# Performance work log

Hardware: AMD Instinct MI355X
Metric: run time of the kernel (lower is better)

The kernel has to match this reference:

```python
import jax, jax.numpy as jnp
import numpy as np

HIDDEN = 20
VOCAB = 29
NUM_LAYERS = 1
SEQ_LEN = 64
BATCH = 16384


def setup_inputs() -> dict:
    key = jax.random.key(0)
    k1, k2, k3, k4, k5 = jax.random.split(key, 5)
    return {
        "x": jax.random.normal(k1, (SEQ_LEN, BATCH, VOCAB), dtype=jnp.float32),
        "img_emb": jax.random.normal(k2, (BATCH, HIDDEN), dtype=jnp.float32),
        "W_ih": jax.random.normal(k3, (NUM_LAYERS, HIDDEN, VOCAB), dtype=jnp.float32),
        "b_ih": jnp.zeros((NUM_LAYERS, HIDDEN), dtype=jnp.float32),
        "W_hh": jax.random.normal(k4, (NUM_LAYERS, HIDDEN, HIDDEN), dtype=jnp.float32),
        "b_hh": jnp.zeros((NUM_LAYERS, HIDDEN), dtype=jnp.float32),
        "W_ho": jax.random.normal(k5, (VOCAB, HIDDEN), dtype=jnp.float32),
        "b_ho": jnp.zeros((VOCAB,), dtype=jnp.float32),
    }


def reference(x, img_emb, W_ih, b_ih, W_hh, b_hh, W_ho, b_ho):
    # num_layers == 1: take layer 0 weights
    Wi, bi = W_ih[0], b_ih[0]   # [H,V], [H]
    Wh, bh = W_hh[0], b_hh[0]   # [H,H], [H]
    seq_len, batch = x.shape[0], x.shape[1]
    # img_emb is only added at t == 0
    first = (jnp.arange(seq_len) == 0).astype(x.dtype)  # [T]

    def step(h, inp):
        xt, f = inp  # xt: [B,V], f: scalar
        h_new = jnp.tanh(xt @ Wi.T + bi + h @ Wh.T + bh + f * img_emb)
        return h_new, h_new

    h0 = jnp.zeros((batch, Wi.shape[0]), dtype=x.dtype)
    _, hs = jax.lax.scan(step, h0, (x, first))  # hs: [T,B,H]
    logits = hs @ W_ho.T + b_ho  # [T,B,V]
    return jax.nn.log_softmax(logits, axis=-1)
```

## Files before the change

kernel.cpp:

```cpp
#include <hip/hip_runtime.h>

#define Tn 64
#define Bn 16384
#define Vn 29
#define Hn 20

typedef float f4 __attribute__((ext_vector_type(4)));

static __device__ __forceinline__ f4 ld4u(const float* p) {
  f4 v; __builtin_memcpy(&v, p, 16); return v;
}
static __device__ __forceinline__ void st4u(float* p, f4 v) {
  __builtin_memcpy(p, &v, 16);
}

#define LOG2E 1.4426950408889634f
#define LN2   0.6931471805599453f

static __device__ __forceinline__ float frcp(float x) {
#if __has_builtin(__builtin_amdgcn_rcpf)
  return __builtin_amdgcn_rcpf(x);
#else
  return 1.0f / x;
#endif
}
static __device__ __forceinline__ float fexp2(float x) {
#if __has_builtin(__builtin_amdgcn_exp2f)
  return __builtin_amdgcn_exp2f(x);
#else
  return exp2f(x);
#endif
}
static __device__ __forceinline__ float flog2(float x) {
#if __has_builtin(__builtin_amdgcn_logf)
  return __builtin_amdgcn_logf(x);
#else
  return log2f(x);
#endif
}
static __device__ __forceinline__ float ftanh(float x) {
  float e = fexp2(x * (2.0f * LOG2E));
  return 1.0f - 2.0f * frcp(1.0f + e);
}

#define SWZ(v, imm) __int_as_float(__builtin_amdgcn_ds_swizzle(__float_as_int(v), (imm)))
#define PAT(ow) (((ow) << 5) | 0x18)

__global__ __launch_bounds__(256, 3) void k_pre(
    const float* __restrict__ x, const float* __restrict__ img,
    const float* __restrict__ Wi, const float* __restrict__ bih,
    const float* __restrict__ bhh, float* __restrict__ xi)
{
  __shared__ f4 sW[Hn * 8];
  __shared__ float sB[Hn];
  float* sWf = (float*)sW;
  const int tid = threadIdx.x;
  for (int i = tid; i < Hn * 32; i += 256) {
    int r = i >> 5, c = i & 31;
    sWf[i] = (c < Vn) ? Wi[r * Vn + c] : 0.0f;
  }
  if (tid < Hn) sB[tid] = bih[tid] + bhh[tid];
  __syncthreads();

  const int g  = blockIdx.x * 256 + tid;
  const int t  = g >> 13;
  const int b0 = (g & 8191) << 1;

  const float* xr = x + ((size_t)t * Bn + b0) * Vn;
  f4 xa[8], xb[8];
#pragma unroll
  for (int q = 0; q < 7; ++q) {
    xa[q] = ld4u(xr + 4 * q);
    xb[q] = ld4u(xr + Vn + 4 * q);
  }
  xa[7] = f4{xr[28], 0.0f, 0.0f, 0.0f};
  xb[7] = f4{xr[Vn + 28], 0.0f, 0.0f, 0.0f};

  const bool first = (t == 0);
  const float* ia = img + (size_t)b0 * Hn;
  float* orow = xi + ((size_t)t * Bn + b0) * Hn;

  float oa4[4], ob4[4];
#pragma unroll
  for (int h = 0; h < Hn; ++h) {
    float aa = sB[h], ab = sB[h];
#pragma unroll
    for (int q = 0; q < 8; ++q) {
      f4 w = sW[h * 8 + q];
      aa += w.x * xa[q].x + w.y * xa[q].y + w.z * xa[q].z + w.w * xa[q].w;
      ab += w.x * xb[q].x + w.y * xb[q].y + w.z * xb[q].z + w.w * xb[q].w;
    }
    if (first) { aa += ia[h]; ab += ia[Hn + h]; }
    oa4[h & 3] = aa; ob4[h & 3] = ab;
    if ((h & 3) == 3) {
      *(f4*)(orow + (h - 3))      = f4{oa4[0], oa4[1], oa4[2], oa4[3]};
      *(f4*)(orow + Hn + (h - 3)) = f4{ob4[0], ob4[1], ob4[2], ob4[3]};
    }
  }
}

__global__ __launch_bounds__(256, 2) void k_rnn(
    const float* __restrict__ xi, const float* __restrict__ Wh,
    const float* __restrict__ Who, const float* __restrict__ bho,
    float* __restrict__ out)
{
  const int gt = blockIdx.x * 256 + threadIdx.x;
  const int b = gt >> 3;
  const int j = gt & 7;

  float wh[3][Hn];
#pragma unroll
  for (int s = 0; s < 3; ++s) {
    int r = 3 * j + s; r = r > 19 ? 19 : r;
    const f4* wr = (const f4*)(Wh + r * Hn);
#pragma unroll
    for (int q = 0; q < 5; ++q) {
      f4 v = wr[q];
      wh[s][4*q] = v.x; wh[s][4*q+1] = v.y; wh[s][4*q+2] = v.z; wh[s][4*q+3] = v.w;
    }
  }
  float wo[4][Hn], bo[4];
#pragma unroll
  for (int rr = 0; rr < 4; ++rr) {
    int v = 4 * j + rr; int vc = v > 28 ? 28 : v;
    const f4* wr = (const f4*)(Who + vc * Hn);
#pragma unroll
    for (int q = 0; q < 5; ++q) {
      f4 w = wr[q];
      wo[rr][4*q] = w.x; wo[rr][4*q+1] = w.y; wo[rr][4*q+2] = w.z; wo[rr][4*q+3] = w.w;
    }
    bo[rr] = (v < Vn) ? bho[v] : -1e30f;
  }

  int c0 = 3 * j;     c0 = c0 > 19 ? 19 : c0;
  int c1 = 3 * j + 1; c1 = c1 > 19 ? 19 : c1;
  int c2 = 3 * j + 2; c2 = c2 > 19 ? 19 : c2;

  const float* xp = xi + (size_t)b * Hn;
  float nx0 = xp[c0], nx1 = xp[c1], nx2 = xp[c2];

  float hbc[Hn];
#pragma unroll
  for (int k = 0; k < Hn; ++k) hbc[k] = 0.0f;

  float* op = out + (size_t)b * Vn + 4 * j;
  const size_t xstep = (size_t)Bn * Hn;
  const size_t ostep = (size_t)Bn * Vn;

#pragma unroll 1
  for (int t = 0; t < Tn; ++t) {
    float a0 = nx0, a1 = nx1, a2 = nx2;
    xp += xstep;
    nx0 = xp[c0]; nx1 = xp[c1]; nx2 = xp[c2];

#pragma unroll
    for (int k = 0; k < Hn; ++k) {
      float hk = hbc[k];
      a0 += hk * wh[0][k]; a1 += hk * wh[1][k]; a2 += hk * wh[2][k];
    }
    float h0 = ftanh(a0), h1 = ftanh(a1), h2 = ftanh(a2);

    hbc[0]  = SWZ(h0, PAT(0)); hbc[1]  = SWZ(h1, PAT(0)); hbc[2]  = SWZ(h2, PAT(0));
    hbc[3]  = SWZ(h0, PAT(1)); hbc[4]  = SWZ(h1, PAT(1)); hbc[5]  = SWZ(h2, PAT(1));
    hbc[6]  = SWZ(h0, PAT(2)); hbc[7]  = SWZ(h1, PAT(2)); hbc[8]  = SWZ(h2, PAT(2));
    hbc[9]  = SWZ(h0, PAT(3)); hbc[10] = SWZ(h1, PAT(3)); hbc[11] = SWZ(h2, PAT(3));
    hbc[12] = SWZ(h0, PAT(4)); hbc[13] = SWZ(h1, PAT(4)); hbc[14] = SWZ(h2, PAT(4));
    hbc[15] = SWZ(h0, PAT(5)); hbc[16] = SWZ(h1, PAT(5)); hbc[17] = SWZ(h2, PAT(5));
    hbc[18] = SWZ(h0, PAT(6)); hbc[19] = SWZ(h1, PAT(6));

    float l0 = bo[0], l1 = bo[1], l2 = bo[2], l3 = bo[3];
#pragma unroll
    for (int k = 0; k < Hn; ++k) {
      float hk = hbc[k];
      l0 += hk * wo[0][k]; l1 += hk * wo[1][k];
      l2 += hk * wo[2][k]; l3 += hk * wo[3][k];
    }

    float m = fmaxf(fmaxf(l0, l1), fmaxf(l2, l3));
    m = fmaxf(m, SWZ(m, 0x041F));
    m = fmaxf(m, SWZ(m, 0x081F));
    m = fmaxf(m, SWZ(m, 0x101F));
    float e0 = fexp2((l0 - m) * LOG2E), e1 = fexp2((l1 - m) * LOG2E);
    float e2 = fexp2((l2 - m) * LOG2E), e3 = fexp2((l3 - m) * LOG2E);
    float s = e0 + e1 + e2 + e3;
    s += SWZ(s, 0x041F);
    s += SWZ(s, 0x081F);
    s += SWZ(s, 0x101F);
    float ls = m + flog2(s) * LN2;

    f4 o = f4{l0 - ls, l1 - ls, l2 - ls, l3 - ls};
    if (j < 7) st4u(op, o);
    else       op[0] = l0 - ls;
    op += ostep;
  }
}

extern "C" void kernel_launch(void* const* d_in, const int* in_sizes, int n_in,
                              void* d_out, int out_size, void* d_ws, size_t ws_size,
                              hipStream_t stream)
{
  const float* x   = (const float*)d_in[0];
  const float* img = (const float*)d_in[1];
  const float* Wi  = (const float*)d_in[2];
  const float* bi  = (const float*)d_in[3];
  const float* Wh  = (const float*)d_in[4];
  const float* bh  = (const float*)d_in[5];
  const float* Who = (const float*)d_in[6];
  const float* bho = (const float*)d_in[7];
  float* out = (float*)d_out;
  float* xi  = (float*)d_ws;

  k_pre<<<(Tn * Bn / 2) / 256, 256, 0, stream>>>(x, img, Wi, bi, bh, xi);
  k_rnn<<<(8 * Bn) / 256, 256, 0, stream>>>(xi, Wh, Who, bho, out);
}
```

Baseline: 316.1 us.

## Fuse input projection into recurrent kernel with prefetched x rows and swizzle broadcast

Removes the separate pre-projection kernel and its workspace round trip. The recurrent kernel now loads raw x rows, with each of the 8 lanes per batch row holding a 4-element slice. It computes x·Wi^T by broadcasting x elements through ds_swizzle, adds the biases and the image embedding at t=0, and prefetches x three steps ahead. This saves writing and rereading the 64×B×20 intermediate, but adds 29 swizzles and 87 FMAs per step on the serial recurrence path, more register pressure (launch bounds lowered to 1), and fewer waves in flight.

```diff
diff --git a/kernel.cpp b/kernel.cpp
--- a/kernel.cpp
+++ b/kernel.cpp
@@ -46,61 +46,31 @@
 #define SWZ(v, imm) __int_as_float(__builtin_amdgcn_ds_swizzle(__float_as_int(v), (imm)))
 #define PAT(ow) (((ow) << 5) | 0x18)
 
-__global__ __launch_bounds__(256, 3) void k_pre(
-    const float* __restrict__ x, const float* __restrict__ img,
-    const float* __restrict__ Wi, const float* __restrict__ bih,
-    const float* __restrict__ bhh, float* __restrict__ xi)
-{
-  __shared__ f4 sW[Hn * 8];
-  __shared__ float sB[Hn];
-  float* sWf = (float*)sW;
-  const int tid = threadIdx.x;
-  for (int i = tid; i < Hn * 32; i += 256) {
-    int r = i >> 5, c = i & 31;
-    sWf[i] = (c < Vn) ? Wi[r * Vn + c] : 0.0f;
-  }
-  if (tid < Hn) sB[tid] = bih[tid] + bhh[tid];
-  __syncthreads();
-
-  const int g  = blockIdx.x * 256 + tid;
-  const int t  = g >> 13;
-  const int b0 = (g & 8191) << 1;
-
-  const float* xr = x + ((size_t)t * Bn + b0) * Vn;
-  f4 xa[8], xb[8];
-#pragma unroll
-  for (int q = 0; q < 7; ++q) {
-    xa[q] = ld4u(xr + 4 * q);
-    xb[q] = ld4u(xr + Vn + 4 * q);
-  }
-  xa[7] = f4{xr[28], 0.0f, 0.0f, 0.0f};
-  xb[7] = f4{xr[Vn + 28], 0.0f, 0.0f, 0.0f};
-
-  const bool first = (t == 0);
-  const float* ia = img + (size_t)b0 * Hn;
-  float* orow = xi + ((size_t)t * Bn + b0) * Hn;
-
-  float oa4[4], ob4[4];
-#pragma unroll
-  for (int h = 0; h < Hn; ++h) {
-    float aa = sB[h], ab = sB[h];
-#pragma unroll
-    for (int q = 0; q < 8; ++q) {
-      f4 w = sW[h * 8 + q];
-      aa += w.x * xa[q].x + w.y * xa[q].y + w.z * xa[q].z + w.w * xa[q].w;
-      ab += w.x * xb[q].x + w.y * xb[q].y + w.z * xb[q].z + w.w * xb[q].w;
-    }
-    if (first) { aa += ia[h]; ab += ia[Hn + h]; }
-    oa4[h & 3] = aa; ob4[h & 3] = ab;
-    if ((h & 3) == 3) {
-      *(f4*)(orow + (h - 3))      = f4{oa4[0], oa4[1], oa4[2], oa4[3]};
-      *(f4*)(orow + Hn + (h - 3)) = f4{ob4[0], ob4[1], ob4[2], ob4[3]};
-    }
-  }
-}
-
-__global__ __launch_bounds__(256, 2) void k_rnn(
-    const float* __restrict__ xi, const float* __restrict__ Wh,
+#define XI_STEP(xv, c) { \
+  float xb_ = SWZ((xv)[(c) & 3], PAT((c) >> 2)); \
+  a0 += wi0[(c)] * xb_; a1 += wi1[(c)] * xb_; a2 += wi2[(c)] * xb_; }
+
+#define XI_ALL(xv) \
+  XI_STEP(xv, 0)  XI_STEP(xv, 1)  XI_STEP(xv, 2)  XI_STEP(xv, 3)  \
+  XI_STEP(xv, 4)  XI_STEP(xv, 5)  XI_STEP(xv, 6)  XI_STEP(xv, 7)  \
+  XI_STEP(xv, 8)  XI_STEP(xv, 9)  XI_STEP(xv, 10) XI_STEP(xv, 11) \
+  XI_STEP(xv, 12) XI_STEP(xv, 13) XI_STEP(xv, 14) XI_STEP(xv, 15) \
+  XI_STEP(xv, 16) XI_STEP(xv, 17) XI_STEP(xv, 18) XI_STEP(xv, 19) \
+  XI_STEP(xv, 20) XI_STEP(xv, 21) XI_STEP(xv, 22) XI_STEP(xv, 23) \
+  XI_STEP(xv, 24) XI_STEP(xv, 25) XI_STEP(xv, 26) XI_STEP(xv, 27) \
+  XI_STEP(xv, 28)
+
+static __device__ __forceinline__ f4 ldx(const float* row, int j) {
+  f4 v;
+  if (j < 7) v = ld4u(row + 4 * j);
+  else       v = f4{row[28], 0.0f, 0.0f, 0.0f};
+  return v;
+}
+
+__global__ __launch_bounds__(256, 1) void k_fused(
+    const float* __restrict__ x,   const float* __restrict__ img,
+    const float* __restrict__ Wi,  const float* __restrict__ bi,
+    const float* __restrict__ Wh,  const float* __restrict__ bh,
     const float* __restrict__ Who, const float* __restrict__ bho,
     float* __restrict__ out)
 {
@@ -108,57 +78,84 @@
   const int b = gt >> 3;
   const int j = gt & 7;
 
-  float wh[3][Hn];
-#pragma unroll
-  for (int s = 0; s < 3; ++s) {
-    int r = 3 * j + s; r = r > 19 ? 19 : r;
-    const f4* wr = (const f4*)(Wh + r * Hn);
-#pragma unroll
-    for (int q = 0; q < 5; ++q) {
-      f4 v = wr[q];
-      wh[s][4*q] = v.x; wh[s][4*q+1] = v.y; wh[s][4*q+2] = v.z; wh[s][4*q+3] = v.w;
-    }
-  }
+  int r0 = 3 * j;     r0 = r0 > 19 ? 19 : r0;
+  int r1 = 3 * j + 1; r1 = r1 > 19 ? 19 : r1;
+  int r2 = 3 * j + 2; r2 = r2 > 19 ? 19 : r2;
+
+  float wi0[Vn], wi1[Vn], wi2[Vn];
+#pragma unroll
+  for (int q = 0; q < 7; ++q) {
+    f4 a = ld4u(Wi + r0 * Vn + 4 * q);
+    f4 c = ld4u(Wi + r1 * Vn + 4 * q);
+    f4 d = ld4u(Wi + r2 * Vn + 4 * q);
+    wi0[4*q]=a.x; wi0[4*q+1]=a.y; wi0[4*q+2]=a.z; wi0[4*q+3]=a.w;
+    wi1[4*q]=c.x; wi1[4*q+1]=c.y; wi1[4*q+2]=c.z; wi1[4*q+3]=c.w;
+    wi2[4*q]=d.x; wi2[4*q+1]=d.y; wi2[4*q+2]=d.z; wi2[4*q+3]=d.w;
+  }
+  wi0[28] = Wi[r0 * Vn + 28];
+  wi1[28] = Wi[r1 * Vn + 28];
+  wi2[28] = Wi[r2 * Vn + 28];
+
+  float wh0[Hn], wh1[Hn], wh2[Hn];
+#pragma unroll
+  for (int q = 0; q < 5; ++q) {
+    f4 a = *(const f4*)(Wh + r0 * Hn + 4 * q);
+    f4 c = *(const f4*)(Wh + r1 * Hn + 4 * q);
+    f4 d = *(const f4*)(Wh + r2 * Hn + 4 * q);
+    wh0[4*q]=a.x; wh0[4*q+1]=a.y; wh0[4*q+2]=a.z; wh0[4*q+3]=a.w;
+    wh1[4*q]=c.x; wh1[4*q+1]=c.y; wh1[4*q+2]=c.z; wh1[4*q+3]=c.w;
+    wh2[4*q]=d.x; wh2[4*q+1]=d.y; wh2[4*q+2]=d.z; wh2[4*q+3]=d.w;
+  }
+
   float wo[4][Hn], bo[4];
 #pragma unroll
   for (int rr = 0; rr < 4; ++rr) {
     int v = 4 * j + rr; int vc = v > 28 ? 28 : v;
-    const f4* wr = (const f4*)(Who + vc * Hn);
 #pragma unroll
     for (int q = 0; q < 5; ++q) {
-      f4 w = wr[q];
-      wo[rr][4*q] = w.x; wo[rr][4*q+1] = w.y; wo[rr][4*q+2] = w.z; wo[rr][4*q+3] = w.w;
+      f4 w = *(const f4*)(Who + vc * Hn + 4 * q);
+      wo[rr][4*q]=w.x; wo[rr][4*q+1]=w.y; wo[rr][4*q+2]=w.z; wo[rr][4*q+3]=w.w;
     }
     bo[rr] = (v < Vn) ? bho[v] : -1e30f;
   }
 
-  int c0 = 3 * j;     c0 = c0 > 19 ? 19 : c0;
-  int c1 = 3 * j + 1; c1 = c1 > 19 ? 19 : c1;
-  int c2 = 3 * j + 2; c2 = c2 > 19 ? 19 : c2;
-
-  const float* xp = xi + (size_t)b * Hn;
-  float nx0 = xp[c0], nx1 = xp[c1], nx2 = xp[c2];
+  const float bs0 = bi[r0] + bh[r0];
+  const float bs1 = bi[r1] + bh[r1];
+  const float bs2 = bi[r2] + bh[r2];
+
+  const size_t S = (size_t)Bn * Vn;
+  const float* xrow = x + (size_t)b * Vn;
+
+  f4 xv = ldx(xrow, j);
+  f4 xA = ldx(xrow + S, j);
+  f4 xB = ldx(xrow + 2 * S, j);
+  const float* pf = xrow + 3 * S;
+
+  float a0 = 0.0f, a1 = 0.0f, a2 = 0.0f;
+  XI_ALL(xv)
+  a0 += bs0 + img[(size_t)b * Hn + r0];
+  a1 += bs1 + img[(size_t)b * Hn + r1];
+  a2 += bs2 + img[(size_t)b * Hn + r2];
 
   float hbc[Hn];
 #pragma unroll
   for (int k = 0; k < Hn; ++k) hbc[k] = 0.0f;
 
   float* op = out + (size_t)b * Vn + 4 * j;
-  const size_t xstep = (size_t)Bn * Hn;
   const size_t ostep = (size_t)Bn * Vn;
 
 #pragma unroll 1
   for (int t = 0; t < Tn; ++t) {
-    float a0 = nx0, a1 = nx1, a2 = nx2;
-    xp += xstep;
-    nx0 = xp[c0]; nx1 = xp[c1]; nx2 = xp[c2];
-
+    f4 xC = ldx(pf, j);
+    if (t < 60) pf += S;
+
+    float A0 = a0, A1 = a1, A2 = a2;
 #pragma unroll
     for (int k = 0; k < Hn; ++k) {
       float hk = hbc[k];
-      a0 += hk * wh[0][k]; a1 += hk * wh[1][k]; a2 += hk * wh[2][k];
+      A0 += hk * wh0[k]; A1 += hk * wh1[k]; A2 += hk * wh2[k];
     }
-    float h0 = ftanh(a0), h1 = ftanh(a1), h2 = ftanh(a2);
+    float h0 = ftanh(A0), h1 = ftanh(A1), h2 = ftanh(A2);
 
     hbc[0]  = SWZ(h0, PAT(0)); hbc[1]  = SWZ(h1, PAT(0)); hbc[2]  = SWZ(h2, PAT(0));
     hbc[3]  = SWZ(h0, PAT(1)); hbc[4]  = SWZ(h1, PAT(1)); hbc[5]  = SWZ(h2, PAT(1));
@@ -192,6 +189,12 @@
     if (j < 7) st4u(op, o);
     else       op[0] = l0 - ls;
     op += ostep;
+
+    a0 = 0.0f; a1 = 0.0f; a2 = 0.0f;
+    XI_ALL(xA)
+    a0 += bs0; a1 += bs1; a2 += bs2;
+
+    xA = xB; xB = xC;
   }
 }
 
@@ -208,8 +211,6 @@
   const float* Who = (const float*)d_in[6];
   const float* bho = (const float*)d_in[7];
   float* out = (float*)d_out;
-  float* xi  = (float*)d_ws;
-
-  k_pre<<<(Tn * Bn / 2) / 256, 256, 0, stream>>>(x, img, Wi, bi, bh, xi);
-  k_rnn<<<(8 * Bn) / 256, 256, 0, stream>>>(xi, Wh, Who, bho, out);
-}
+
+  k_fused<<<(8 * Bn) / 256, 256, 0, stream>>>(x, img, Wi, bi, Wh, bh, Who, bho, out);
+}
```

Result: slower. 390.3 us (+23.5%).
